# Performance work log

Hardware: AMD Instinct MI355X
Metric: run time of the kernel (lower is better)

## Reference

```python
import jax, jax.numpy as jnp
import numpy as np
import math

D_MODEL = 1024
NUM_HEADS = 16
HEAD_DIM = D_MODEL // NUM_HEADS
BATCH = 2
SEQ = 2048
THETA = 10000.0


def _rope_tables(seq_len, head_dim, theta=THETA):
    inv_freq = 1.0 / theta ** (jnp.arange(0, head_dim, 2, dtype=jnp.float32) / head_dim)
    pos = jnp.arange(seq_len, dtype=jnp.float32)
    freqs = jnp.outer(pos, inv_freq)                 # [S, hd/2]
    emb = jnp.concatenate([freqs, freqs], axis=-1)   # [S, hd]
    return jnp.cos(emb), jnp.sin(emb)


def _rotate_half(x):
    x1, x2 = jnp.split(x, 2, axis=-1)
    return jnp.concatenate([-x2, x1], axis=-1)


def setup_inputs() -> dict:
    key = jax.random.key(0)
    k1, k2, k3 = jax.random.split(key, 3)
    x = jax.random.normal(k1, (BATCH, SEQ, D_MODEL), dtype=jnp.float32)
    # causal mask: 1 where attend allowed, 0 where masked
    mask = jnp.tril(jnp.ones((SEQ, SEQ), dtype=jnp.int32))[None, None]
    w_qkv = jax.random.normal(k2, (D_MODEL, 3 * D_MODEL), dtype=jnp.float32) / math.sqrt(D_MODEL)
    w_out = jax.random.normal(k3, (D_MODEL, D_MODEL), dtype=jnp.float32) / math.sqrt(D_MODEL)
    return {"x": x, "mask": mask, "w_qkv": w_qkv, "w_out": w_out}


def reference(x, mask, w_qkv, w_out):
    B, S, _ = x.shape
    qkv = x @ w_qkv                                          # [B,S,3*D]
    qkv = qkv.reshape(B, S, 3, NUM_HEADS, HEAD_DIM)
    qkv = jnp.transpose(qkv, (2, 0, 3, 1, 4))                # [3,B,H,S,hd]
    q, k, v = qkv[0], qkv[1], qkv[2]
    cos, sin = _rope_tables(S, HEAD_DIM)                     # [S,hd]
    cos = cos[None, None]; sin = sin[None, None]
    q = q * cos + _rotate_half(q) * sin
    k = k * cos + _rotate_half(k) * sin
    scores = jnp.einsum('bhqd,bhkd->bhqk', q, k) / math.sqrt(HEAD_DIM)
    scores = jnp.where(mask == 0, -jnp.inf, scores)
    attn = jax.nn.softmax(scores, axis=-1)                   # dropout p=0 (eval)
    out = jnp.einsum('bhqk,bhkd->bhqd', attn, v)             # [B,H,S,hd]
    out = jnp.transpose(out, (0, 2, 1, 3)).reshape(B, S, D_MODEL)
    return out @ w_out
```

## Files before the change

### kernel.cpp

```cpp
#include <hip/hip_runtime.h>

typedef __bf16 bf16;
typedef __bf16 bf16x4 __attribute__((ext_vector_type(4)));
typedef __bf16 bf16x8 __attribute__((ext_vector_type(8)));
typedef short s16x4 __attribute__((ext_vector_type(4)));
typedef float f32x4 __attribute__((ext_vector_type(4)));

constexpr int BATCH = 2;
constexpr int SEQ   = 2048;
constexpr int DMODEL= 1024;
constexpr int NH    = 16;
constexpr int HD    = 64;
constexpr int M_ROWS= BATCH * SEQ;
constexpr int N_QKV = 3 * DMODEL;

__device__ __forceinline__ void gl_lds16(const bf16* g, bf16* l) {
  __builtin_amdgcn_global_load_lds(
      (const __attribute__((address_space(1))) unsigned int*)g,
      (__attribute__((address_space(3))) unsigned int*)l, 16, 0, 0);
}

__device__ __forceinline__ f32x4 mfma_16x16x16_bf16(bf16x4 a, bf16x4 b,
                                                    f32x4 c) {
#if defined(__HIP_DEVICE_COMPILE__)
  union { bf16x4 h; s16x4 s; } ua{a}, ub{b};
  return __builtin_amdgcn_mfma_f32_16x16x16bf16_1k(ua.s, ub.s, c, 0, 0, 0);
#else
  return c;
#endif
}

__global__ __launch_bounds__(256) void transpose_cast_kernel(
    const float* __restrict__ src, bf16* __restrict__ dst, int R, int C) {
  __shared__ float tile[32][33];
  const int c0 = blockIdx.x * 32, r0 = blockIdx.y * 32;
  const int tx = threadIdx.x, ty = threadIdx.y;
#pragma unroll
  for (int i = 0; i < 4; i++)
    tile[ty + 8 * i][tx] = src[(size_t)(r0 + ty + 8 * i) * C + c0 + tx];
  __syncthreads();
#pragma unroll
  for (int i = 0; i < 4; i++)
    dst[(size_t)(c0 + ty + 8 * i) * R + r0 + tx] = (bf16)tile[tx][ty + 8 * i];
}

__global__ __launch_bounds__(256) void cast_f32_bf16(
    const float* __restrict__ src, bf16* __restrict__ dst) {
  const int i = (blockIdx.x * 256 + threadIdx.x) * 8;
  float4 f0 = *(const float4*)&src[i];
  float4 f1 = *(const float4*)&src[i + 4];
  bf16x8 v;
  v[0] = (bf16)f0.x; v[1] = (bf16)f0.y; v[2] = (bf16)f0.z; v[3] = (bf16)f0.w;
  v[4] = (bf16)f1.x; v[5] = (bf16)f1.y; v[6] = (bf16)f1.z; v[7] = (bf16)f1.w;
  *(bf16x8*)&dst[i] = v;
}

#define GEMM_BODY(A, BT, K)                                                    \
  __shared__ bf16 As[128 * 32];                                                \
  __shared__ bf16 Bs[128 * 32];                                                \
  const int t = threadIdx.x;                                                   \
  const int m0 = blockIdx.y * 128;                                             \
  const int n0 = blockIdx.x * 128;                                             \
  const int w = t >> 6, lane = t & 63, g = lane >> 4, li = lane & 15;          \
  const int r0w = (w & 1) * 64, c0w = (w >> 1) * 64;                           \
  f32x4 acc[4][4] = {};                                                        \
  for (int k0 = 0; k0 < (K); k0 += 32) {                                       \
    __syncthreads();                                                           \
    _Pragma("unroll") for (int c = 0; c < 2; c++) {                            \
      const int idx = (w * 2 + c) * 64 + lane;                                 \
      const int row = idx >> 2, col = (idx & 3) * 8;                           \
      gl_lds16(&(A)[(size_t)(m0 + row) * (K) + k0 + col],                      \
               &As[(w * 2 + c) * 512]);                                        \
      gl_lds16(&(BT)[(size_t)(n0 + row) * (K) + k0 + col],                     \
               &Bs[(w * 2 + c) * 512]);                                        \
    }                                                                          \
    __syncthreads();                                                           \
    bf16x8 a[4], b[4];                                                         \
    _Pragma("unroll") for (int mt = 0; mt < 4; mt++)                           \
        a[mt] = *(const bf16x8*)&As[(r0w + mt * 16 + li) * 32 + g * 8];        \
    _Pragma("unroll") for (int nt = 0; nt < 4; nt++)                           \
        b[nt] = *(const bf16x8*)&Bs[(c0w + nt * 16 + li) * 32 + g * 8];        \
    _Pragma("unroll") for (int mt = 0; mt < 4; mt++)                           \
        _Pragma("unroll") for (int nt = 0; nt < 4; nt++)                       \
            acc[mt][nt] = __builtin_amdgcn_mfma_f32_16x16x32_bf16(             \
                a[mt], b[nt], acc[mt][nt], 0, 0, 0);                           \
  }

__global__ __launch_bounds__(256) void gemm_out(
    const bf16* __restrict__ A, const bf16* __restrict__ BT,
    float* __restrict__ C, int M, int N, int K) {
  GEMM_BODY(A, BT, K)
#pragma unroll
  for (int mt = 0; mt < 4; mt++)
#pragma unroll
    for (int nt = 0; nt < 4; nt++)
#pragma unroll
      for (int r = 0; r < 4; r++) {
        const int m = m0 + r0w + mt * 16 + g * 4 + r;
        const int n = n0 + c0w + nt * 16 + li;
        C[(size_t)m * N + n] = acc[mt][nt][r];
      }
}

__global__ __launch_bounds__(256) void gemm_qkv_rope(
    const bf16* __restrict__ A, const bf16* __restrict__ BT,
    bf16* __restrict__ Qb, bf16* __restrict__ Kb, bf16* __restrict__ Vt) {
  constexpr int K = DMODEL;
  GEMM_BODY(A, BT, K)

  const int region = n0 >> 10;
  const int b = m0 >> 11;
  const int h = ((n0 + c0w) >> 6) & 15;
  const size_t bh = (size_t)(b * NH + h);

  if (region < 2) {
    bf16* dst = region == 0 ? Qb : Kb;
    const float outsc = region == 0 ? 0.125f * 1.44269504f : 1.f;
    const float L = 13.287712379549449f;
    const float if0 = exp2f(-(float)(2 * li) / 64.f * L);
    const float if1 = exp2f(-(float)(2 * (li + 16)) / 64.f * L);
#pragma unroll
    for (int mt = 0; mt < 4; mt++)
#pragma unroll
      for (int r = 0; r < 4; r++) {
        const int s = (m0 + r0w + mt * 16 + g * 4 + r) & (SEQ - 1);
        float cs[2], sn[2];
        __sincosf((float)s * if0, &sn[0], &cs[0]);
        __sincosf((float)s * if1, &sn[1], &cs[1]);
#pragma unroll
        for (int nt = 0; nt < 4; nt++) {
          const int d = nt * 16 + li;
          const int par = nt & 1;
          const float a = acc[mt][nt][r];
          const float ap = acc[mt][nt ^ 2][r];
          const float v = (nt < 2) ? a * cs[par] - ap * sn[par]
                                   : a * cs[par] + ap * sn[par];
          dst[(bh * SEQ + s) * HD + d] = (bf16)(v * outsc);
        }
      }
  } else {
#pragma unroll
    for (int mt = 0; mt < 4; mt++)
#pragma unroll
      for (int nt = 0; nt < 4; nt++) {
        const int s = (m0 + r0w + mt * 16 + g * 4) & (SEQ - 1);
        const int d = nt * 16 + li;
        bf16x4 v;
#pragma unroll
        for (int r = 0; r < 4; r++) v[r] = (bf16)acc[mt][nt][r];
        *(bf16x4*)&Vt[(bh * HD + d) * SEQ + s] = v;
      }
  }
}

__global__ __launch_bounds__(256, 4) void flash_attn8(
    const bf16* __restrict__ Q, const bf16* __restrict__ Kb,
    const bf16* __restrict__ Vt, bf16* __restrict__ Oout) {
  const int bx = blockIdx.x;
  const int qt = 31 - (bx >> 5);
  const int bh = bx & 31;
  const int q0 = qt * 64;
  const int t = threadIdx.x, w = t >> 6, lane = t & 63, g = lane >> 4,
            li = lane & 15;

  __shared__ bf16 Ks[2][4096];
  __shared__ bf16 Vs[2][4096];

  const bf16* Qh = Q  + (size_t)bh * SEQ * HD;
  const bf16* Kh = Kb + (size_t)bh * SEQ * HD;
  const bf16* Vh = Vt + (size_t)bh * HD * SEQ;

  const int qw = q0 + w * 16;

  bf16x8 qf[2];
#pragma unroll
  for (int ks = 0; ks < 2; ks++)
    qf[ks] = *(const bf16x8*)&Qh[(size_t)(qw + li) * HD + ks * 32 + g * 8];

  f32x4 o[4] = {};
  f32x4 o4  = {};
  bf16x4 ones;
#pragma unroll
  for (int r = 0; r < 4; r++) ones[r] = (bf16)1.f;

  const int p0 = w * 128 + lane, p1 = p0 + 64;
  const int sr0 = p0 >> 3, sc0 = ((p0 & 7) ^ (sr0 & 7)) * 8;
  const int sr1 = p1 >> 3, sc1 = ((p1 & 7) ^ (sr1 & 7)) * 8;
  const int lo0 = w * 1024, lo1 = w * 1024 + 512;

  const int jend = q0 + 64;

  gl_lds16(&Kh[(size_t)sr0 * HD + sc0], &Ks[0][lo0]);
  gl_lds16(&Kh[(size_t)sr1 * HD + sc1], &Ks[0][lo1]);
  gl_lds16(&Vh[(size_t)sr0 * SEQ + sc0], &Vs[0][lo0]);
  gl_lds16(&Vh[(size_t)sr1 * SEQ + sc1], &Vs[0][lo1]);
  __syncthreads();

  for (int j0 = 0; j0 < jend; j0 += 64) {
    const int cur = (j0 >> 6) & 1, nxt = cur ^ 1;
    if (j0 + 64 < jend) {
      const int jn = j0 + 64;
      gl_lds16(&Kh[(size_t)(jn + sr0) * HD + sc0], &Ks[nxt][lo0]);
      gl_lds16(&Kh[(size_t)(jn + sr1) * HD + sc1], &Ks[nxt][lo1]);
      gl_lds16(&Vh[(size_t)sr0 * SEQ + jn + sc0], &Vs[nxt][lo0]);
      gl_lds16(&Vh[(size_t)sr1 * SEQ + jn + sc1], &Vs[nxt][lo1]);
    }

    if (j0 <= qw + 15) {
      const bool masked = (j0 + 63 > qw);
      const int ntlim = min(4, ((qw + 15 - j0) >> 4) + 1);

      f32x4 sacc[4] = {};
#pragma unroll
      for (int ks = 0; ks < 2; ks++)
#pragma unroll
        for (int nt = 0; nt < 4; nt++) {
          if (nt >= ntlim) continue;
          const int rK = nt * 16 + li;
          const int pK = rK * 8 + ((ks * 4 + g) ^ (li & 7));
          bf16x8 kf = *(const bf16x8*)&Ks[cur][pK * 8];
          sacc[nt] = __builtin_amdgcn_mfma_f32_16x16x32_bf16(kf, qf[ks],
                                                             sacc[nt], 0, 0, 0);
        }

      bf16x4 pf[4];
#pragma unroll
      for (int nt = 0; nt < 4; nt++) {
        if (nt >= ntlim) continue;
#pragma unroll
        for (int r = 0; r < 4; r++) {
          float v = sacc[nt][r];
          if (masked) {
            const int kk = j0 + nt * 16 + g * 4 + r;
            v = (kk <= qw + li) ? v : -1e30f;
          }
          pf[nt][r] = (bf16)exp2f(v);
        }
      }

#pragma unroll
      for (int nt = 0; nt < 4; nt++) {
        if (nt >= ntlim) continue;
        o4 = mfma_16x16x16_bf16(ones, pf[nt], o4);
#pragma unroll
        for (int dt = 0; dt < 4; dt++) {
          const int rV = dt * 16 + li;
          const int cg = nt * 2 + (g >> 1);
          const int pV = rV * 8 + (cg ^ (rV & 7));
          bf16x4 vfrag = *(const bf16x4*)&Vs[cur][pV * 8 + (g & 1) * 4];
          o[dt] = mfma_16x16x16_bf16(vfrag, pf[nt], o[dt]);
        }
      }
    }
    __syncthreads();
  }

  const float inv_l = 1.f / o4[0];

  const int b = bh >> 4, h = bh & 15;
  const int s = qw + li;
#pragma unroll
  for (int dt = 0; dt < 4; dt++) {
    bf16x4 ov;
#pragma unroll
    for (int r = 0; r < 4; r++) ov[r] = (bf16)(o[dt][r] * inv_l);
    *(bf16x4*)&Oout[((size_t)(b * SEQ + s)) * DMODEL + h * 64 + dt * 16 +
                    g * 4] = ov;
  }
}

extern "C" void kernel_launch(void* const* d_in, const int* in_sizes, int n_in,
                              void* d_out, int out_size, void* d_ws,
                              size_t ws_size, hipStream_t stream) {
  const float* x     = (const float*)d_in[0];
  const float* w_qkv = (const float*)d_in[2];
  const float* w_out = (const float*)d_in[3];
  float* out = (float*)d_out;

  char* ws = (char*)d_ws;
  bf16* WqkvT = (bf16*)(ws);
  bf16* WoutT = (bf16*)(ws + 6291456);
  bf16* xb    = (bf16*)(ws + 8388608);
  bf16* Qb    = (bf16*)(ws + 16777216);
  bf16* Kbuf  = (bf16*)(ws + 25165824);
  bf16* Vt    = (bf16*)(ws + 33554432);
  bf16* attn  = (bf16*)(ws + 41943040);

  cast_f32_bf16<<<M_ROWS * DMODEL / 2048, 256, 0, stream>>>(x, xb);
  transpose_cast_kernel<<<dim3(N_QKV / 32, DMODEL / 32), dim3(32, 8), 0,
                          stream>>>(w_qkv, WqkvT, DMODEL, N_QKV);
  transpose_cast_kernel<<<dim3(DMODEL / 32, DMODEL / 32), dim3(32, 8), 0,
                          stream>>>(w_out, WoutT, DMODEL, DMODEL);
  gemm_qkv_rope<<<dim3(N_QKV / 128, M_ROWS / 128), 256, 0, stream>>>(
      xb, WqkvT, Qb, Kbuf, Vt);
  flash_attn8<<<dim3(1024), 256, 0, stream>>>(Qb, Kbuf, Vt, attn);
  gemm_out<<<dim3(DMODEL / 128, M_ROWS / 128), 256, 0, stream>>>(
      attn, WoutT, out, M_ROWS, DMODEL, DMODEL);
}
```

Baseline: 212.0 us.

## Split causal attention over key chunks with atomic fp32 accumulation and normalize pass

The attention kernel now gives each block a query tile plus a chunk of at most 256 keys, using a triangular index mapping over 4608 blocks instead of one block per query tile walking the whole causal prefix. Partial unnormalized outputs and row sums go into fp32 buffers with atomic adds. A new normalize kernel divides by the row sum and writes the bf16 head-interleaved output. The aim is to remove the load imbalance of long causal rows and raise parallelism. In exchange it adds two memsets, 16 MB of fp32 atomic traffic and an extra launch, and Lsum reuses the x bf16 workspace region.

```diff
diff --git a/kernel.cpp b/kernel.cpp
--- a/kernel.cpp
+++ b/kernel.cpp
@@ -153,13 +153,29 @@
   }
 }
 
-__global__ __launch_bounds__(256, 4) void flash_attn8(
+__global__ __launch_bounds__(256, 4) void flash_attn9(
     const bf16* __restrict__ Q, const bf16* __restrict__ Kb,
-    const bf16* __restrict__ Vt, bf16* __restrict__ Oout) {
+    const bf16* __restrict__ Vt, float* __restrict__ Ofp,
+    float* __restrict__ Lsum) {
   const int bx = blockIdx.x;
-  const int qt = 31 - (bx >> 5);
   const int bh = bx & 31;
+  const int z = bx >> 5;
+  int a = 0;
+#pragma unroll
+  for (int i = 0; i < 7; i++)
+    if (z >= 2 * (a + 1) * (a + 2)) a++;
+  const int rem = z - 2 * a * (a + 1);
+  const int ap1 = a + 1;
+  const int bq = (rem >= 3 * ap1) ? 3 : (rem >= 2 * ap1) ? 2
+                 : (rem >= ap1)   ? 1 : 0;
+  const int c0 = rem - bq * ap1;
+  const int qt = 4 * a + bq;
+
   const int q0 = qt * 64;
+  const int j0s = c0 * 256;
+  const int jendv = min(j0s + 256, q0 + 64);
+  const int ntiles = (jendv - j0s) >> 6;
+
   const int t = threadIdx.x, w = t >> 6, lane = t & 63, g = lane >> 4,
             li = lane & 15;
 
@@ -188,17 +204,16 @@
   const int sr1 = p1 >> 3, sc1 = ((p1 & 7) ^ (sr1 & 7)) * 8;
   const int lo0 = w * 1024, lo1 = w * 1024 + 512;
 
-  const int jend = q0 + 64;
-
-  gl_lds16(&Kh[(size_t)sr0 * HD + sc0], &Ks[0][lo0]);
-  gl_lds16(&Kh[(size_t)sr1 * HD + sc1], &Ks[0][lo1]);
-  gl_lds16(&Vh[(size_t)sr0 * SEQ + sc0], &Vs[0][lo0]);
-  gl_lds16(&Vh[(size_t)sr1 * SEQ + sc1], &Vs[0][lo1]);
+  gl_lds16(&Kh[(size_t)(j0s + sr0) * HD + sc0], &Ks[0][lo0]);
+  gl_lds16(&Kh[(size_t)(j0s + sr1) * HD + sc1], &Ks[0][lo1]);
+  gl_lds16(&Vh[(size_t)sr0 * SEQ + j0s + sc0], &Vs[0][lo0]);
+  gl_lds16(&Vh[(size_t)sr1 * SEQ + j0s + sc1], &Vs[0][lo1]);
   __syncthreads();
 
-  for (int j0 = 0; j0 < jend; j0 += 64) {
-    const int cur = (j0 >> 6) & 1, nxt = cur ^ 1;
-    if (j0 + 64 < jend) {
+  for (int i = 0; i < ntiles; i++) {
+    const int j0 = j0s + i * 64;
+    const int cur = i & 1, nxt = cur ^ 1;
+    if (i + 1 < ntiles) {
       const int jn = j0 + 64;
       gl_lds16(&Kh[(size_t)(jn + sr0) * HD + sc0], &Ks[nxt][lo0]);
       gl_lds16(&Kh[(size_t)(jn + sr1) * HD + sc1], &Ks[nxt][lo1]);
@@ -206,67 +221,80 @@
       gl_lds16(&Vh[(size_t)sr1 * SEQ + jn + sc1], &Vs[nxt][lo1]);
     }
 
-    if (j0 <= qw + 15) {
-      const bool masked = (j0 + 63 > qw);
-      const int ntlim = min(4, ((qw + 15 - j0) >> 4) + 1);
-
-      f32x4 sacc[4] = {};
-#pragma unroll
-      for (int ks = 0; ks < 2; ks++)
-#pragma unroll
-        for (int nt = 0; nt < 4; nt++) {
-          if (nt >= ntlim) continue;
-          const int rK = nt * 16 + li;
-          const int pK = rK * 8 + ((ks * 4 + g) ^ (li & 7));
-          bf16x8 kf = *(const bf16x8*)&Ks[cur][pK * 8];
-          sacc[nt] = __builtin_amdgcn_mfma_f32_16x16x32_bf16(kf, qf[ks],
-                                                             sacc[nt], 0, 0, 0);
-        }
-
-      bf16x4 pf[4];
+    const bool masked = (j0 + 63 > qw);
+    const int ntlim = min(4, ((qw + 15 - j0) >> 4) + 1);
+
+    f32x4 sacc[4] = {};
+#pragma unroll
+    for (int ks = 0; ks < 2; ks++)
 #pragma unroll
       for (int nt = 0; nt < 4; nt++) {
         if (nt >= ntlim) continue;
-#pragma unroll
-        for (int r = 0; r < 4; r++) {
-          float v = sacc[nt][r];
-          if (masked) {
-            const int kk = j0 + nt * 16 + g * 4 + r;
-            v = (kk <= qw + li) ? v : -1e30f;
-          }
-          pf[nt][r] = (bf16)exp2f(v);
+        const int rK = nt * 16 + li;
+        const int pK = rK * 8 + ((ks * 4 + g) ^ (li & 7));
+        bf16x8 kf = *(const bf16x8*)&Ks[cur][pK * 8];
+        sacc[nt] = __builtin_amdgcn_mfma_f32_16x16x32_bf16(kf, qf[ks],
+                                                           sacc[nt], 0, 0, 0);
+      }
+
+    bf16x4 pf[4];
+#pragma unroll
+    for (int nt = 0; nt < 4; nt++) {
+      if (nt >= ntlim) continue;
+#pragma unroll
+      for (int r = 0; r < 4; r++) {
+        float v = sacc[nt][r];
+        if (masked) {
+          const int kk = j0 + nt * 16 + g * 4 + r;
+          v = (kk <= qw + li) ? v : -1e30f;
         }
-      }
-
-#pragma unroll
-      for (int nt = 0; nt < 4; nt++) {
-        if (nt >= ntlim) continue;
-        o4 = mfma_16x16x16_bf16(ones, pf[nt], o4);
-#pragma unroll
-        for (int dt = 0; dt < 4; dt++) {
-          const int rV = dt * 16 + li;
-          const int cg = nt * 2 + (g >> 1);
-          const int pV = rV * 8 + (cg ^ (rV & 7));
-          bf16x4 vfrag = *(const bf16x4*)&Vs[cur][pV * 8 + (g & 1) * 4];
-          o[dt] = mfma_16x16x16_bf16(vfrag, pf[nt], o[dt]);
-        }
+        pf[nt][r] = (bf16)exp2f(v);
+      }
+    }
+
+#pragma unroll
+    for (int nt = 0; nt < 4; nt++) {
+      if (nt >= ntlim) continue;
+      o4 = mfma_16x16x16_bf16(ones, pf[nt], o4);
+#pragma unroll
+      for (int dt = 0; dt < 4; dt++) {
+        const int rV = dt * 16 + li;
+        const int cg = nt * 2 + (g >> 1);
+        const int pV = rV * 8 + (cg ^ (rV & 7));
+        bf16x4 vfrag = *(const bf16x4*)&Vs[cur][pV * 8 + (g & 1) * 4];
+        o[dt] = mfma_16x16x16_bf16(vfrag, pf[nt], o[dt]);
       }
     }
     __syncthreads();
   }
 
-  const float inv_l = 1.f / o4[0];
-
+  const size_t obase = ((size_t)bh * SEQ + qw + li) * HD;
+#pragma unroll
+  for (int dt = 0; dt < 4; dt++)
+#pragma unroll
+    for (int r = 0; r < 4; r++)
+      unsafeAtomicAdd(&Ofp[obase + dt * 16 + g * 4 + r], o[dt][r]);
+  if (g == 0) unsafeAtomicAdd(&Lsum[bh * SEQ + qw + li], o4[0]);
+}
+
+__global__ __launch_bounds__(256) void attn_normalize(
+    const float* __restrict__ Ofp, const float* __restrict__ Lsum,
+    bf16* __restrict__ attn) {
+  const int tid = blockIdx.x * 256 + threadIdx.x;
+  const int dvg = tid & 7;
+  const int q   = (tid >> 3) & (SEQ - 1);
+  const int bh  = tid >> 14;
+  const float inv_l = 1.f / Lsum[bh * SEQ + q];
+  const float* src = &Ofp[((size_t)bh * SEQ + q) * HD + dvg * 8];
+  float4 f0 = *(const float4*)src;
+  float4 f1 = *(const float4*)(src + 4);
+  bf16x8 v;
+  v[0] = (bf16)(f0.x * inv_l); v[1] = (bf16)(f0.y * inv_l);
+  v[2] = (bf16)(f0.z * inv_l); v[3] = (bf16)(f0.w * inv_l);
+  v[4] = (bf16)(f1.x * inv_l); v[5] = (bf16)(f1.y * inv_l);
+  v[6] = (bf16)(f1.z * inv_l); v[7] = (bf16)(f1.w * inv_l);
   const int b = bh >> 4, h = bh & 15;
-  const int s = qw + li;
-#pragma unroll
-  for (int dt = 0; dt < 4; dt++) {
-    bf16x4 ov;
-#pragma unroll
-    for (int r = 0; r < 4; r++) ov[r] = (bf16)(o[dt][r] * inv_l);
-    *(bf16x4*)&Oout[((size_t)(b * SEQ + s)) * DMODEL + h * 64 + dt * 16 +
-                    g * 4] = ov;
-  }
+  *(bf16x8*)&attn[((size_t)(b * SEQ + q)) * DMODEL + h * 64 + dvg * 8] = v;
 }
 
 extern "C" void kernel_launch(void* const* d_in, const int* in_sizes, int n_in,
@@ -278,13 +306,15 @@
   float* out = (float*)d_out;
 
   char* ws = (char*)d_ws;
-  bf16* WqkvT = (bf16*)(ws);
-  bf16* WoutT = (bf16*)(ws + 6291456);
-  bf16* xb    = (bf16*)(ws + 8388608);
-  bf16* Qb    = (bf16*)(ws + 16777216);
-  bf16* Kbuf  = (bf16*)(ws + 25165824);
-  bf16* Vt    = (bf16*)(ws + 33554432);
-  bf16* attn  = (bf16*)(ws + 41943040);
+  bf16*  WqkvT = (bf16*)(ws);
+  bf16*  WoutT = (bf16*)(ws + 6291456);
+  bf16*  xb    = (bf16*)(ws + 8388608);
+  float* Lsum  = (float*)(ws + 8388608);
+  bf16*  Qb    = (bf16*)(ws + 16777216);
+  bf16*  Kbuf  = (bf16*)(ws + 25165824);
+  bf16*  Vt    = (bf16*)(ws + 33554432);
+  bf16*  attn  = (bf16*)(ws + 41943040);
+  float* Ofp   = (float*)(ws + 50331648);
 
   cast_f32_bf16<<<M_ROWS * DMODEL / 2048, 256, 0, stream>>>(x, xb);
   transpose_cast_kernel<<<dim3(N_QKV / 32, DMODEL / 32), dim3(32, 8), 0,
@@ -293,7 +323,10 @@
                           stream>>>(w_out, WoutT, DMODEL, DMODEL);
   gemm_qkv_rope<<<dim3(N_QKV / 128, M_ROWS / 128), 256, 0, stream>>>(
       xb, WqkvT, Qb, Kbuf, Vt);
-  flash_attn8<<<dim3(1024), 256, 0, stream>>>(Qb, Kbuf, Vt, attn);
+  hipMemsetAsync(Ofp, 0, 16777216, stream);
+  hipMemsetAsync(Lsum, 0, 262144, stream);
+  flash_attn9<<<dim3(4608), 256, 0, stream>>>(Qb, Kbuf, Vt, Ofp, Lsum);
+  attn_normalize<<<dim3(2048), 256, 0, stream>>>(Ofp, Lsum, attn);
   gemm_out<<<dim3(DMODEL / 128, M_ROWS / 128), 256, 0, stream>>>(
       attn, WoutT, out, M_ROWS, DMODEL, DMODEL);
 }
```

New measurement: 411.4 us. +94.1%, slower.

## Pair causal query tiles per attention block and shrink output GEMM row tile

Applied to the files above, without the earlier changes.

The attention kernel now processes two query tiles per block, one short and one long causal range (pr and 31-pr), so every block does equal work, halving the grid and relaxing launch bounds. The output projection GEMM switches to 64x128 tiles, doubling block count to fill more compute units. The intent is to reduce load imbalance and tail effects; the trade-offs are less parallelism in attention and lower per-block data reuse in the GEMM.

```diff
diff --git a/kernel.cpp b/kernel.cpp
--- a/kernel.cpp
+++ b/kernel.cpp
@@ -86,12 +86,47 @@
                 a[mt], b[nt], acc[mt][nt], 0, 0, 0);                           \
   }
 
-__global__ __launch_bounds__(256) void gemm_out(
+__global__ __launch_bounds__(256) void gemm_out64(
     const bf16* __restrict__ A, const bf16* __restrict__ BT,
     float* __restrict__ C, int M, int N, int K) {
-  GEMM_BODY(A, BT, K)
-#pragma unroll
-  for (int mt = 0; mt < 4; mt++)
+  __shared__ bf16 As[64 * 32];
+  __shared__ bf16 Bs[128 * 32];
+  const int t = threadIdx.x;
+  const int m0 = blockIdx.y * 64;
+  const int n0 = blockIdx.x * 128;
+  const int w = t >> 6, lane = t & 63, g = lane >> 4, li = lane & 15;
+  const int r0w = (w & 1) * 32, c0w = (w >> 1) * 64;
+  f32x4 acc[2][4] = {};
+  for (int k0 = 0; k0 < K; k0 += 32) {
+    __syncthreads();
+    {
+      const int idx = w * 64 + lane;
+      const int row = idx >> 2, col = (idx & 3) * 8;
+      gl_lds16(&A[(size_t)(m0 + row) * K + k0 + col], &As[w * 512]);
+    }
+#pragma unroll
+    for (int c = 0; c < 2; c++) {
+      const int idx = (w * 2 + c) * 64 + lane;
+      const int row = idx >> 2, col = (idx & 3) * 8;
+      gl_lds16(&BT[(size_t)(n0 + row) * K + k0 + col], &Bs[(w * 2 + c) * 512]);
+    }
+    __syncthreads();
+    bf16x8 a[2], b[4];
+#pragma unroll
+    for (int mt = 0; mt < 2; mt++)
+      a[mt] = *(const bf16x8*)&As[(r0w + mt * 16 + li) * 32 + g * 8];
+#pragma unroll
+    for (int nt = 0; nt < 4; nt++)
+      b[nt] = *(const bf16x8*)&Bs[(c0w + nt * 16 + li) * 32 + g * 8];
+#pragma unroll
+    for (int mt = 0; mt < 2; mt++)
+#pragma unroll
+      for (int nt = 0; nt < 4; nt++)
+        acc[mt][nt] = __builtin_amdgcn_mfma_f32_16x16x32_bf16(
+            a[mt], b[nt], acc[mt][nt], 0, 0, 0);
+  }
+#pragma unroll
+  for (int mt = 0; mt < 2; mt++)
 #pragma unroll
     for (int nt = 0; nt < 4; nt++)
 #pragma unroll
@@ -153,13 +188,12 @@
   }
 }
 
-__global__ __launch_bounds__(256, 4) void flash_attn8(
+__global__ __launch_bounds__(256, 2) void flash_attn10(
     const bf16* __restrict__ Q, const bf16* __restrict__ Kb,
     const bf16* __restrict__ Vt, bf16* __restrict__ Oout) {
   const int bx = blockIdx.x;
-  const int qt = 31 - (bx >> 5);
   const int bh = bx & 31;
-  const int q0 = qt * 64;
+  const int pr = bx >> 5;
   const int t = threadIdx.x, w = t >> 6, lane = t & 63, g = lane >> 4,
             li = lane & 15;
 
@@ -169,16 +203,8 @@
   const bf16* Qh = Q  + (size_t)bh * SEQ * HD;
   const bf16* Kh = Kb + (size_t)bh * SEQ * HD;
   const bf16* Vh = Vt + (size_t)bh * HD * SEQ;
-
-  const int qw = q0 + w * 16;
-
-  bf16x8 qf[2];
-#pragma unroll
-  for (int ks = 0; ks < 2; ks++)
-    qf[ks] = *(const bf16x8*)&Qh[(size_t)(qw + li) * HD + ks * 32 + g * 8];
-
-  f32x4 o[4] = {};
-  f32x4 o4  = {};
+  const int b = bh >> 4, h = bh & 15;
+
   bf16x4 ones;
 #pragma unroll
   for (int r = 0; r < 4; r++) ones[r] = (bf16)1.f;
@@ -188,84 +214,95 @@
   const int sr1 = p1 >> 3, sc1 = ((p1 & 7) ^ (sr1 & 7)) * 8;
   const int lo0 = w * 1024, lo1 = w * 1024 + 512;
 
-  const int jend = q0 + 64;
-
-  gl_lds16(&Kh[(size_t)sr0 * HD + sc0], &Ks[0][lo0]);
-  gl_lds16(&Kh[(size_t)sr1 * HD + sc1], &Ks[0][lo1]);
-  gl_lds16(&Vh[(size_t)sr0 * SEQ + sc0], &Vs[0][lo0]);
-  gl_lds16(&Vh[(size_t)sr1 * SEQ + sc1], &Vs[0][lo1]);
-  __syncthreads();
-
-  for (int j0 = 0; j0 < jend; j0 += 64) {
-    const int cur = (j0 >> 6) & 1, nxt = cur ^ 1;
-    if (j0 + 64 < jend) {
-      const int jn = j0 + 64;
-      gl_lds16(&Kh[(size_t)(jn + sr0) * HD + sc0], &Ks[nxt][lo0]);
-      gl_lds16(&Kh[(size_t)(jn + sr1) * HD + sc1], &Ks[nxt][lo1]);
-      gl_lds16(&Vh[(size_t)sr0 * SEQ + jn + sc0], &Vs[nxt][lo0]);
-      gl_lds16(&Vh[(size_t)sr1 * SEQ + jn + sc1], &Vs[nxt][lo1]);
-    }
-
-    if (j0 <= qw + 15) {
-      const bool masked = (j0 + 63 > qw);
-      const int ntlim = min(4, ((qw + 15 - j0) >> 4) + 1);
-
-      f32x4 sacc[4] = {};
-#pragma unroll
-      for (int ks = 0; ks < 2; ks++)
+  for (int seg = 0; seg < 2; seg++) {
+    const int qt = seg ? 31 - pr : pr;
+    const int q0 = qt * 64;
+    const int qw = q0 + w * 16;
+    const int jend = q0 + 64;
+
+    bf16x8 qf[2];
+#pragma unroll
+    for (int ks = 0; ks < 2; ks++)
+      qf[ks] = *(const bf16x8*)&Qh[(size_t)(qw + li) * HD + ks * 32 + g * 8];
+
+    f32x4 o[4] = {};
+    f32x4 o4  = {};
+
+    gl_lds16(&Kh[(size_t)sr0 * HD + sc0], &Ks[0][lo0]);
+    gl_lds16(&Kh[(size_t)sr1 * HD + sc1], &Ks[0][lo1]);
+    gl_lds16(&Vh[(size_t)sr0 * SEQ + sc0], &Vs[0][lo0]);
+    gl_lds16(&Vh[(size_t)sr1 * SEQ + sc1], &Vs[0][lo1]);
+    __syncthreads();
+
+    for (int j0 = 0; j0 < jend; j0 += 64) {
+      const int cur = (j0 >> 6) & 1, nxt = cur ^ 1;
+      if (j0 + 64 < jend) {
+        const int jn = j0 + 64;
+        gl_lds16(&Kh[(size_t)(jn + sr0) * HD + sc0], &Ks[nxt][lo0]);
+        gl_lds16(&Kh[(size_t)(jn + sr1) * HD + sc1], &Ks[nxt][lo1]);
+        gl_lds16(&Vh[(size_t)sr0 * SEQ + jn + sc0], &Vs[nxt][lo0]);
+        gl_lds16(&Vh[(size_t)sr1 * SEQ + jn + sc1], &Vs[nxt][lo1]);
+      }
+
+      if (j0 <= qw + 15) {
+        const bool masked = (j0 + 63 > qw);
+        const int ntlim = min(4, ((qw + 15 - j0) >> 4) + 1);
+
+        f32x4 sacc[4] = {};
+#pragma unroll
+        for (int ks = 0; ks < 2; ks++)
+#pragma unroll
+          for (int nt = 0; nt < 4; nt++) {
+            if (nt >= ntlim) continue;
+            const int rK = nt * 16 + li;
+            const int pK = rK * 8 + ((ks * 4 + g) ^ (li & 7));
+            bf16x8 kf = *(const bf16x8*)&Ks[cur][pK * 8];
+            sacc[nt] = __builtin_amdgcn_mfma_f32_16x16x32_bf16(
+                kf, qf[ks], sacc[nt], 0, 0, 0);
+          }
+
+        bf16x4 pf[4];
 #pragma unroll
         for (int nt = 0; nt < 4; nt++) {
           if (nt >= ntlim) continue;
-          const int rK = nt * 16 + li;
-          const int pK = rK * 8 + ((ks * 4 + g) ^ (li & 7));
-          bf16x8 kf = *(const bf16x8*)&Ks[cur][pK * 8];
-          sacc[nt] = __builtin_amdgcn_mfma_f32_16x16x32_bf16(kf, qf[ks],
-                                                             sacc[nt], 0, 0, 0);
+#pragma unroll
+          for (int r = 0; r < 4; r++) {
+            float v = sacc[nt][r];
+            if (masked) {
+              const int kk = j0 + nt * 16 + g * 4 + r;
+              v = (kk <= qw + li) ? v : -1e30f;
+            }
+            pf[nt][r] = (bf16)exp2f(v);
+          }
         }
 
-      bf16x4 pf[4];
-#pragma unroll
-      for (int nt = 0; nt < 4; nt++) {
-        if (nt >= ntlim) continue;
-#pragma unroll
-        for (int r = 0; r < 4; r++) {
-          float v = sacc[nt][r];
-          if (masked) {
-            const int kk = j0 + nt * 16 + g * 4 + r;
-            v = (kk <= qw + li) ? v : -1e30f;
+#pragma unroll
+        for (int nt = 0; nt < 4; nt++) {
+          if (nt >= ntlim) continue;
+          o4 = mfma_16x16x16_bf16(ones, pf[nt], o4);
+#pragma unroll
+          for (int dt = 0; dt < 4; dt++) {
+            const int rV = dt * 16 + li;
+            const int cg = nt * 2 + (g >> 1);
+            const int pV = rV * 8 + (cg ^ (rV & 7));
+            bf16x4 vfrag = *(const bf16x4*)&Vs[cur][pV * 8 + (g & 1) * 4];
+            o[dt] = mfma_16x16x16_bf16(vfrag, pf[nt], o[dt]);
           }
-          pf[nt][r] = (bf16)exp2f(v);
         }
       }
-
-#pragma unroll
-      for (int nt = 0; nt < 4; nt++) {
-        if (nt >= ntlim) continue;
-        o4 = mfma_16x16x16_bf16(ones, pf[nt], o4);
-#pragma unroll
-        for (int dt = 0; dt < 4; dt++) {
-          const int rV = dt * 16 + li;
-          const int cg = nt * 2 + (g >> 1);
-          const int pV = rV * 8 + (cg ^ (rV & 7));
-          bf16x4 vfrag = *(const bf16x4*)&Vs[cur][pV * 8 + (g & 1) * 4];
-          o[dt] = mfma_16x16x16_bf16(vfrag, pf[nt], o[dt]);
-        }
-      }
+      __syncthreads();
     }
-    __syncthreads();
-  }
-
-  const float inv_l = 1.f / o4[0];
-
-  const int b = bh >> 4, h = bh & 15;
-  const int s = qw + li;
-#pragma unroll
-  for (int dt = 0; dt < 4; dt++) {
-    bf16x4 ov;
-#pragma unroll
-    for (int r = 0; r < 4; r++) ov[r] = (bf16)(o[dt][r] * inv_l);
-    *(bf16x4*)&Oout[((size_t)(b * SEQ + s)) * DMODEL + h * 64 + dt * 16 +
-                    g * 4] = ov;
+
+    const float inv_l = 1.f / o4[0];
+    const int s = qw + li;
+#pragma unroll
+    for (int dt = 0; dt < 4; dt++) {
+      bf16x4 ov;
+#pragma unroll
+      for (int r = 0; r < 4; r++) ov[r] = (bf16)(o[dt][r] * inv_l);
+      *(bf16x4*)&Oout[((size_t)(b * SEQ + s)) * DMODEL + h * 64 + dt * 16 +
+                      g * 4] = ov;
+    }
   }
 }
 
@@ -293,7 +330,7 @@
                           stream>>>(w_out, WoutT, DMODEL, DMODEL);
   gemm_qkv_rope<<<dim3(N_QKV / 128, M_ROWS / 128), 256, 0, stream>>>(
       xb, WqkvT, Qb, Kbuf, Vt);
-  flash_attn8<<<dim3(1024), 256, 0, stream>>>(Qb, Kbuf, Vt, attn);
-  gemm_out<<<dim3(DMODEL / 128, M_ROWS / 128), 256, 0, stream>>>(
+  flash_attn10<<<dim3(512), 256, 0, stream>>>(Qb, Kbuf, Vt, attn);
+  gemm_out64<<<dim3(DMODEL / 128, M_ROWS / 64), 256, 0, stream>>>(
       attn, WoutT, out, M_ROWS, DMODEL, DMODEL);
 }
```

Result: slower. 221.5 us (+4.5%).
